# Kernel optimization log

Hardware: AMD Instinct MI355X
Metric: run time of the kernel (lower is better)

Reference implementation:

```python
import jax, jax.numpy as jnp
import numpy as np

N = 50000
IN_DIM = 2000
GRAPH_DIM = 512
HIDDEN_DIM = 256
LATENT_DIM = 64
N_EDGES = 1600000
BN_EPS = 1e-5


def setup_inputs() -> dict:
    key = jax.random.key(0)
    ks = jax.random.split(key, 12)
    x = jax.random.normal(ks[0], (N, IN_DIM), dtype=jnp.float32)
    adj_rows = jax.random.randint(ks[1], (N_EDGES,), 0, N, dtype=jnp.int32)
    adj_cols = jax.random.randint(ks[2], (N_EDGES,), 0, N, dtype=jnp.int32)
    adj_vals = jax.random.uniform(ks[3], (N_EDGES,), dtype=jnp.float32)
    def xavier(k, fan_in, fan_out):
        lim = np.sqrt(6.0 / (fan_in + fan_out)).astype(np.float32)
        return jax.random.uniform(k, (fan_in, fan_out), minval=-lim, maxval=lim, dtype=jnp.float32)
    Wg = xavier(ks[4], IN_DIM, GRAPH_DIM)
    bg = jnp.zeros((GRAPH_DIM,), jnp.float32)
    W1 = xavier(ks[5], GRAPH_DIM, HIDDEN_DIM)
    b1 = jnp.zeros((HIDDEN_DIM,), jnp.float32)
    W21 = xavier(ks[6], HIDDEN_DIM, LATENT_DIM)
    b21 = jnp.zeros((LATENT_DIM,), jnp.float32)
    W22 = xavier(ks[7], HIDDEN_DIM, LATENT_DIM)
    b22 = jnp.zeros((LATENT_DIM,), jnp.float32)
    gamma0 = jnp.ones((GRAPH_DIM,), jnp.float32)
    beta0 = jnp.zeros((GRAPH_DIM,), jnp.float32)
    gamma1 = jnp.ones((HIDDEN_DIM,), jnp.float32)
    beta1 = jnp.zeros((HIDDEN_DIM,), jnp.float32)
    return {"x": x, "adj_rows": adj_rows, "adj_cols": adj_cols, "adj_vals": adj_vals,
            "Wg": Wg, "bg": bg, "W1": W1, "b1": b1, "W21": W21, "b21": b21,
            "W22": W22, "b22": b22, "gamma0": gamma0, "beta0": beta0,
            "gamma1": gamma1, "beta1": beta1}


def batchnorm(h, gamma, beta):
    # training-mode BatchNorm1d: biased variance over batch (node) dim
    mean = jnp.mean(h, axis=0)
    var = jnp.var(h, axis=0)
    return (h - mean) * jax.lax.rsqrt(var + BN_EPS) * gamma + beta


def reference(x, adj_rows, adj_cols, adj_vals, Wg, bg, W1, b1, W21, b21, W22, b22,
              gamma0, beta0, gamma1, beta1):
    # GCN layer: dense projection then sparse aggregation (SpMM via segment_sum)
    h = x @ Wg + bg                                   # [N, GRAPH_DIM]
    msgs = adj_vals[:, None] * h[adj_cols]            # [E, GRAPH_DIM]
    agg = jax.ops.segment_sum(msgs, adj_rows, num_segments=N)
    h0 = jax.nn.softplus(batchnorm(agg, gamma0, beta0))
    h1 = jax.nn.softplus(batchnorm(h0 @ W1 + b1, gamma1, beta1))
    mu = h1 @ W21 + b21
    logvar = h1 @ W22 + b22
    return (mu, logvar)
```

## Files before the change

kernel.cpp:

```cpp
#include <hip/hip_runtime.h>
#include <hip/hip_bf16.h>
#include <stdint.h>

typedef __attribute__((ext_vector_type(8))) short short8;
typedef __attribute__((ext_vector_type(8))) unsigned short ushort8;
typedef __attribute__((ext_vector_type(4))) float f32x4;

#define DEVFN static __device__ __forceinline__

#define NNODES 50000
#define MPAD   50048
#define EDGES  1600000

DEVFN float bf2f(unsigned short u){
  unsigned int v = ((unsigned int)u) << 16;
  return __builtin_bit_cast(float, v);
}
DEVFN unsigned short f2bf(float f){
  unsigned int u = __builtin_bit_cast(unsigned int, f);
  u += 0x7FFFu + ((u >> 16) & 1u);
  return (unsigned short)(u >> 16);
}

typedef __attribute__((address_space(1))) const unsigned int gu32_t;
typedef __attribute__((address_space(3))) unsigned int lu32_t;
DEVFN void async16(const void* g, void* l){
  __builtin_amdgcn_global_load_lds((gu32_t*)g, (lu32_t*)l, 16, 0, 0);
}

__global__ void cast_x_kernel(const float* __restrict__ x, unsigned short* __restrict__ xb){
  long i = (long)blockIdx.x * blockDim.x + threadIdx.x;
  const long total = (long)MPAD * 2048 / 8;
  const long stride = (long)gridDim.x * blockDim.x;
  for (; i < total; i += stride){
    long e0 = i * 8;
    int row = (int)(e0 >> 11);
    int col = (int)(e0 & 2047);
    ushort8 v = {0,0,0,0,0,0,0,0};
    if (row < NNODES && col < 2000){
      const float* s = x + (long)row * 2000 + col;
      #pragma unroll
      for (int j = 0; j < 8; j++) v[j] = f2bf(s[j]);
    }
    *(ushort8*)(xb + e0) = v;
  }
}

__global__ void transpose_cast(const float* __restrict__ src, unsigned short* __restrict__ dst,
                               int K, int Ncols, int Kpad, int rowOff){
  long i = (long)blockIdx.x * blockDim.x + threadIdx.x;
  long total = (long)Ncols * Kpad;
  long stride = (long)gridDim.x * blockDim.x;
  for (; i < total; i += stride){
    int n = (int)(i / Kpad);
    int k = (int)(i - (long)n * Kpad);
    unsigned short v = 0;
    if (k < K) v = f2bf(src[(long)k * Ncols + n]);
    dst[(long)(rowOff + n) * Kpad + k] = v;
  }
}

__global__ void hist_kernel(const int* __restrict__ rows, int* __restrict__ counts){
  int i = blockIdx.x * blockDim.x + threadIdx.x;
  int stride = gridDim.x * blockDim.x;
  for (; i < EDGES; i += stride) atomicAdd(&counts[rows[i]], 1);
}

__global__ void scan_kernel(const int* __restrict__ counts, int* __restrict__ offs){
  __shared__ int part[1024];
  const int n = NNODES;
  const int chunk = 49;
  int t = threadIdx.x;
  int base = t * chunk;
  int s = 0;
  for (int i = 0; i < chunk; i++){ int idx = base + i; if (idx < n) s += counts[idx]; }
  part[t] = s; __syncthreads();
  for (int off = 1; off < 1024; off <<= 1){
    int v = 0;
    if (t >= off) v = part[t - off];
    __syncthreads();
    part[t] += v;
    __syncthreads();
  }
  int run = t ? part[t - 1] : 0;
  for (int i = 0; i < chunk; i++){
    int idx = base + i;
    if (idx <= n){
      offs[idx] = run;
      if (idx < n) run += counts[idx];
    }
  }
}

__global__ void fill_kernel(const int* __restrict__ rows, const int* __restrict__ cols,
                            const float* __restrict__ vals, int* __restrict__ cursor,
                            int* __restrict__ ecol, float* __restrict__ eval){
  int i = blockIdx.x * blockDim.x + threadIdx.x;
  int stride = gridDim.x * blockDim.x;
  for (; i < EDGES; i += stride){
    int r = rows[i];
    int p = atomicAdd(&cursor[r], 1);
    ecol[p] = cols[i];
    eval[p] = vals[i];
  }
}

__launch_bounds__(256)
__global__ void aggregate_kernel(const int* __restrict__ offs, const int* __restrict__ ecol,
                                 const float* __restrict__ eval, const unsigned short* __restrict__ h,
                                 float* __restrict__ agg){
  int wv = threadIdx.x >> 6, lane = threadIdx.x & 63;
  int node = blockIdx.x * 4 + wv;
  int beg = offs[node], end = offs[node + 1];
  float acc[8];
  #pragma unroll
  for (int j = 0; j < 8; j++) acc[j] = 0.f;
  const unsigned short* hp = h + lane * 8;
  for (int i = beg; i < end; i++){
    int c = ecol[i];
    float v = eval[i];
    ushort8 u = *(const ushort8*)(hp + (long)c * 512);
    #pragma unroll
    for (int j = 0; j < 8; j++) acc[j] = fmaf(v, bf2f(u[j]), acc[j]);
  }
  float* op = agg + (long)node * 512 + lane * 8;
  f32x4 lo = {acc[0], acc[1], acc[2], acc[3]};
  f32x4 hi = {acc[4], acc[5], acc[6], acc[7]};
  *(f32x4*)op = lo;
  *(f32x4*)(op + 4) = hi;
}

template<int C>
__global__ void bn_stats_kernel(const float* __restrict__ z, double* __restrict__ dsum, double* __restrict__ dsq){
  constexpr int PC = C / 256;
  int t = threadIdx.x;
  float s[PC], q[PC];
  #pragma unroll
  for (int p = 0; p < PC; p++){ s[p] = 0.f; q[p] = 0.f; }
  for (int r = blockIdx.x; r < NNODES; r += gridDim.x){
    const float* zr = z + (long)r * C;
    #pragma unroll
    for (int p = 0; p < PC; p++){
      float v = zr[t + p * 256];
      s[p] += v; q[p] += v * v;
    }
  }
  #pragma unroll
  for (int p = 0; p < PC; p++){
    atomicAdd(&dsum[t + p * 256], (double)s[p]);
    atomicAdd(&dsq[t + p * 256], (double)q[p]);
  }
}

__global__ void bn_finalize_kernel(const double* __restrict__ dsum, const double* __restrict__ dsq,
                                   const float* __restrict__ gamma, const float* __restrict__ beta,
                                   float* __restrict__ scale, float* __restrict__ shift, int C){
  int c = blockIdx.x * blockDim.x + threadIdx.x;
  if (c < C){
    double m = dsum[c] / (double)NNODES;
    double var = dsq[c] / (double)NNODES - m * m;
    float rs = (float)(1.0 / sqrt(var + 1e-5));
    float sc = rs * gamma[c];
    scale[c] = sc;
    shift[c] = beta[c] - (float)m * sc;
  }
}

template<int C>
__global__ void bn_softplus_kernel(const float* __restrict__ z, const float* __restrict__ scale,
                                   const float* __restrict__ shift, unsigned short* __restrict__ out,
                                   int rowsTotal){
  long i = (long)blockIdx.x * blockDim.x + threadIdx.x;
  long total = (long)rowsTotal * C / 8;
  long stride = (long)gridDim.x * blockDim.x;
  for (; i < total; i += stride){
    long e0 = i * 8;
    int c0 = (int)(e0 & (C - 1));
    const float* zp = z + e0;
    ushort8 o;
    #pragma unroll
    for (int j = 0; j < 8; j++){
      float y = fmaf(zp[j], scale[c0 + j], shift[c0 + j]);
      float sp = (y > 15.f) ? y : log1pf(__expf(y));
      o[j] = f2bf(sp);
    }
    *(ushort8*)(out + e0) = o;
  }
}

template<int EPI>
__launch_bounds__(256, 2)
__global__ void gemm_kernel(const unsigned short* __restrict__ A, const unsigned short* __restrict__ B,
                            const float* __restrict__ bias, const float* __restrict__ bias2,
                            void* __restrict__ Cout, int N, int K){
  __shared__ unsigned short As[128 * 64];
  __shared__ unsigned short Bs[128 * 64];
  const int t = threadIdx.x;
  const int lane = t & 63;
  const int w = t >> 6;
  const long row0 = (long)blockIdx.x * 128;
  const int col0 = blockIdx.y * 128;

  const int rI = lane >> 3;
  const int sI = (lane & 7) ^ rI;

  f32x4 acc[4][4];
  #pragma unroll
  for (int i = 0; i < 4; i++)
    #pragma unroll
    for (int j = 0; j < 4; j++){
      f32x4 z = {0.f, 0.f, 0.f, 0.f};
      acc[i][j] = z;
    }

  const int wm = (w >> 1) * 64;
  const int wn = (w & 1) * 64;
  const int nk = K >> 6;

  const unsigned short* Abase = A + row0 * K + sI * 8;
  const unsigned short* Bbase = B + (long)col0 * K + sI * 8;

  for (int kt = 0; kt < nk; ++kt){
    const int kb = kt * 64;
    #pragma unroll
    for (int i = 0; i < 4; i++){
      int c = i * 4 + w;
      int rowt = c * 8 + rI;
      async16(Abase + (long)rowt * K + kb, As + c * 512);
      async16(Bbase + (long)rowt * K + kb, Bs + c * 512);
    }
    __syncthreads();
    #pragma unroll
    for (int ks = 0; ks < 2; ++ks){
      short8 af[4], bfr[4];
      #pragma unroll
      for (int f = 0; f < 4; f++){
        int ra = wm + f * 16 + (lane & 15);
        int sa = (ks * 4 + (lane >> 4)) ^ (ra & 7);
        af[f] = *(const short8*)(As + ra * 64 + sa * 8);
        int rb = wn + f * 16 + (lane & 15);
        int sb = (ks * 4 + (lane >> 4)) ^ (rb & 7);
        bfr[f] = *(const short8*)(Bs + rb * 64 + sb * 8);
      }
      #pragma unroll
      for (int fm = 0; fm < 4; fm++)
        #pragma unroll
        for (int fn = 0; fn < 4; fn++)
          acc[fm][fn] = __builtin_amdgcn_mfma_f32_16x16x32_bf16(af[fm], bfr[fn], acc[fm][fn], 0, 0, 0);
    }
    __syncthreads();
  }

  #pragma unroll
  for (int fm = 0; fm < 4; fm++){
    #pragma unroll
    for (int fn = 0; fn < 4; fn++){
      #pragma unroll
      for (int j = 0; j < 4; j++){
        long r = row0 + wm + fm * 16 + ((lane >> 4) * 4 + j);
        int cc = col0 + wn + fn * 16 + (lane & 15);
        float v = acc[fm][fn][j];
        if (EPI == 0){
          v += bias[cc];
          ((unsigned short*)Cout)[r * N + cc] = f2bf(v);
        } else if (EPI == 1){
          v += bias[cc];
          ((float*)Cout)[r * N + cc] = v;
        } else {
          if (r < NNODES){
            float bb = (cc < 64) ? bias[cc] : bias2[cc - 64];
            long o = (cc < 64) ? ((long)r * 64 + cc) : ((long)64 * NNODES + (long)r * 64 + (cc - 64));
            ((float*)Cout)[o] = v + bb;
          }
        }
      }
    }
  }
}

extern "C" void kernel_launch(void* const* d_in, const int* in_sizes, int n_in,
                              void* d_out, int out_size, void* d_ws, size_t ws_size,
                              hipStream_t stream){
  const float* x        = (const float*)d_in[0];
  const int*   adj_rows = (const int*)d_in[1];
  const int*   adj_cols = (const int*)d_in[2];
  const float* adj_vals = (const float*)d_in[3];
  const float* Wg       = (const float*)d_in[4];
  const float* bg       = (const float*)d_in[5];
  const float* W1       = (const float*)d_in[6];
  const float* b1       = (const float*)d_in[7];
  const float* W21      = (const float*)d_in[8];
  const float* b21      = (const float*)d_in[9];
  const float* W22      = (const float*)d_in[10];
  const float* b22      = (const float*)d_in[11];
  const float* gamma0   = (const float*)d_in[12];
  const float* beta0    = (const float*)d_in[13];
  const float* gamma1   = (const float*)d_in[14];
  const float* beta1    = (const float*)d_in[15];

  char* ws = (char*)d_ws;
  unsigned short* xb  = (unsigned short*)(ws + 0);
  float* agg          = (float*)(ws + 0);
  float* z1           = (float*)(ws + 102498304);
  unsigned short* h1  = (unsigned short*)(ws + 153747456);
  size_t o = 205000704;
  unsigned short* WgT = (unsigned short*)(ws + o); o += 2097152;
  unsigned short* W1T = (unsigned short*)(ws + o); o += 262144;
  unsigned short* WcT = (unsigned short*)(ws + o); o += 65536;
  unsigned short* hbf = (unsigned short*)(ws + o); o += 51249152;
  unsigned short* h0  = (unsigned short*)(ws + o); o += 51249152;
  int* counts = (int*)(ws + o); o += 200192;
  int* offs   = (int*)(ws + o); o += 200192;
  int* cursor = (int*)(ws + o); o += 200192;
  int* ecol   = (int*)(ws + o); o += 6400000;
  float* eval = (float*)(ws + o); o += 6400000;
  double* dsum0 = (double*)(ws + o); o += 4096;
  double* dsq0  = (double*)(ws + o); o += 4096;
  double* dsum1 = (double*)(ws + o); o += 2048;
  double* dsq1  = (double*)(ws + o); o += 2048;
  float* scale0 = (float*)(ws + o); o += 2048;
  float* shift0 = (float*)(ws + o); o += 2048;
  float* scale1 = (float*)(ws + o); o += 1024;
  float* shift1 = (float*)(ws + o); o += 1024;

  hipMemsetAsync(counts, 0, NNODES * sizeof(int), stream);
  hipMemsetAsync(dsum0, 0, 12288, stream);

  cast_x_kernel<<<2048, 256, 0, stream>>>(x, xb);
  transpose_cast<<<512, 256, 0, stream>>>(Wg, WgT, 2000, 512, 2048, 0);
  transpose_cast<<<128, 256, 0, stream>>>(W1, W1T, 512, 256, 512, 0);
  transpose_cast<<<64, 256, 0, stream>>>(W21, WcT, 256, 64, 256, 0);
  transpose_cast<<<64, 256, 0, stream>>>(W22, WcT, 256, 64, 256, 64);

  hist_kernel<<<2048, 256, 0, stream>>>(adj_rows, counts);
  scan_kernel<<<1, 1024, 0, stream>>>(counts, offs);
  hipMemcpyAsync(cursor, offs, NNODES * sizeof(int), hipMemcpyDeviceToDevice, stream);
  fill_kernel<<<2048, 256, 0, stream>>>(adj_rows, adj_cols, adj_vals, cursor, ecol, eval);

  gemm_kernel<0><<<dim3(MPAD / 128, 4), 256, 0, stream>>>(xb, WgT, bg, nullptr, hbf, 512, 2048);

  aggregate_kernel<<<NNODES / 4, 256, 0, stream>>>(offs, ecol, eval, hbf, agg);

  bn_stats_kernel<512><<<512, 256, 0, stream>>>(agg, dsum0, dsq0);
  bn_finalize_kernel<<<2, 256, 0, stream>>>(dsum0, dsq0, gamma0, beta0, scale0, shift0, 512);
  bn_softplus_kernel<512><<<2048, 256, 0, stream>>>(agg, scale0, shift0, h0, MPAD);

  gemm_kernel<1><<<dim3(MPAD / 128, 2), 256, 0, stream>>>(h0, W1T, b1, nullptr, z1, 256, 512);

  bn_stats_kernel<256><<<512, 256, 0, stream>>>(z1, dsum1, dsq1);
  bn_finalize_kernel<<<1, 256, 0, stream>>>(dsum1, dsq1, gamma1, beta1, scale1, shift1, 256);
  bn_softplus_kernel<256><<<1024, 256, 0, stream>>>(z1, scale1, shift1, h1, MPAD);

  gemm_kernel<2><<<dim3(MPAD / 128, 1), 256, 0, stream>>>(h1, WcT, b21, b22, (float*)d_out, 128, 256);

  (void)in_sizes; (void)n_in; (void)out_size; (void)ws_size;
}
```

Measured before the change: 1.579 ms.

## Parallelize CSR scan, pack edges, unroll aggregation, fuse weight prep

The single-block serial scan becomes a three-kernel parallel scan that also writes the cursor, which removes the device-to-device memcpy. Edge column and value are packed into one 64-bit word, and the aggregation loop is unrolled by four so that four row gathers are in flight at once. The four weight transpose launches are fused into one kernel, and softplus uses a cheaper stable fast-math form. The cost is two extra small scan launches, and the fast log/exp intrinsics give slightly lower precision.

Result: faster. 1.319 ms (-16.4%).

```diff
diff --git a/kernel.cpp b/kernel.cpp
--- a/kernel.cpp
+++ b/kernel.cpp
@@ -11,6 +11,7 @@
 #define NNODES 50000
 #define MPAD   50048
 #define EDGES  1600000
+#define SCHUNK 196
 
 DEVFN float bf2f(unsigned short u){
   unsigned int v = ((unsigned int)u) << 16;
@@ -46,17 +47,33 @@
   }
 }
 
-__global__ void transpose_cast(const float* __restrict__ src, unsigned short* __restrict__ dst,
-                               int K, int Ncols, int Kpad, int rowOff){
-  long i = (long)blockIdx.x * blockDim.x + threadIdx.x;
-  long total = (long)Ncols * Kpad;
-  long stride = (long)gridDim.x * blockDim.x;
+__global__ void prep_weights(const float* __restrict__ Wg, const float* __restrict__ W1,
+                             const float* __restrict__ W21, const float* __restrict__ W22,
+                             unsigned short* __restrict__ WgT, unsigned short* __restrict__ W1T,
+                             unsigned short* __restrict__ WcT){
+  const int n0 = 512 * 2048;
+  const int n1 = 256 * 512;
+  const int n2 = 64 * 256;
+  const int total = n0 + n1 + 2 * n2;
+  int i = blockIdx.x * blockDim.x + threadIdx.x;
+  int stride = gridDim.x * blockDim.x;
   for (; i < total; i += stride){
-    int n = (int)(i / Kpad);
-    int k = (int)(i - (long)n * Kpad);
-    unsigned short v = 0;
-    if (k < K) v = f2bf(src[(long)k * Ncols + n]);
-    dst[(long)(rowOff + n) * Kpad + k] = v;
+    if (i < n0){
+      int n = i >> 11, k = i & 2047;
+      WgT[i] = (k < 2000) ? f2bf(Wg[(long)k * 512 + n]) : (unsigned short)0;
+    } else if (i < n0 + n1){
+      int j = i - n0;
+      int n = j >> 9, k = j & 511;
+      W1T[j] = f2bf(W1[(long)k * 256 + n]);
+    } else if (i < n0 + n1 + n2){
+      int j = i - n0 - n1;
+      int n = j >> 8, k = j & 255;
+      WcT[j] = f2bf(W21[(long)k * 64 + n]);
+    } else {
+      int j = i - n0 - n1 - n2;
+      int n = j >> 8, k = j & 255;
+      WcT[n2 + j] = f2bf(W22[(long)k * 64 + n]);
+    }
   }
 }
 
@@ -66,49 +83,68 @@
   for (; i < EDGES; i += stride) atomicAdd(&counts[rows[i]], 1);
 }
 
-__global__ void scan_kernel(const int* __restrict__ counts, int* __restrict__ offs){
-  __shared__ int part[1024];
-  const int n = NNODES;
-  const int chunk = 49;
+__global__ void scan_partials(const int* __restrict__ counts, int* __restrict__ part){
+  __shared__ int red[256];
+  int b = blockIdx.x, t = threadIdx.x;
+  int idx = b * SCHUNK + t;
+  int s = (t < SCHUNK && idx < NNODES) ? counts[idx] : 0;
+  red[t] = s; __syncthreads();
+  for (int o = 128; o; o >>= 1){
+    if (t < o) red[t] += red[t + o];
+    __syncthreads();
+  }
+  if (!t) part[b] = red[0];
+}
+
+__global__ void scan_scan(int* __restrict__ part){
+  __shared__ int s[256];
   int t = threadIdx.x;
-  int base = t * chunk;
-  int s = 0;
-  for (int i = 0; i < chunk; i++){ int idx = base + i; if (idx < n) s += counts[idx]; }
-  part[t] = s; __syncthreads();
-  for (int off = 1; off < 1024; off <<= 1){
-    int v = 0;
-    if (t >= off) v = part[t - off];
-    __syncthreads();
-    part[t] += v;
-    __syncthreads();
-  }
-  int run = t ? part[t - 1] : 0;
-  for (int i = 0; i < chunk; i++){
-    int idx = base + i;
-    if (idx <= n){
-      offs[idx] = run;
-      if (idx < n) run += counts[idx];
-    }
+  s[t] = part[t]; __syncthreads();
+  for (int o = 1; o < 256; o <<= 1){
+    int v = (t >= o) ? s[t - o] : 0;
+    __syncthreads();
+    s[t] += v;
+    __syncthreads();
+  }
+  part[t] = t ? s[t - 1] : 0;
+}
+
+__global__ void scan_expand(const int* __restrict__ counts, const int* __restrict__ part,
+                            int* __restrict__ offs, int* __restrict__ cursor){
+  __shared__ int s[256];
+  int b = blockIdx.x, t = threadIdx.x;
+  int idx = b * SCHUNK + t;
+  int val = (t < SCHUNK && idx < NNODES) ? counts[idx] : 0;
+  s[t] = val; __syncthreads();
+  for (int o = 1; o < 256; o <<= 1){
+    int v = (t >= o) ? s[t - o] : 0;
+    __syncthreads();
+    s[t] += v;
+    __syncthreads();
+  }
+  if (t < SCHUNK && idx <= NNODES){
+    int excl = s[t] - val + part[b];
+    if (idx < NNODES){ offs[idx] = excl; cursor[idx] = excl; }
+    else offs[NNODES] = excl;
   }
 }
 
 __global__ void fill_kernel(const int* __restrict__ rows, const int* __restrict__ cols,
                             const float* __restrict__ vals, int* __restrict__ cursor,
-                            int* __restrict__ ecol, float* __restrict__ eval){
+                            unsigned long long* __restrict__ ep){
   int i = blockIdx.x * blockDim.x + threadIdx.x;
   int stride = gridDim.x * blockDim.x;
   for (; i < EDGES; i += stride){
     int r = rows[i];
     int p = atomicAdd(&cursor[r], 1);
-    ecol[p] = cols[i];
-    eval[p] = vals[i];
+    unsigned int vb = __builtin_bit_cast(unsigned int, vals[i]);
+    ep[p] = ((unsigned long long)vb << 32) | (unsigned int)cols[i];
   }
 }
 
 __launch_bounds__(256)
-__global__ void aggregate_kernel(const int* __restrict__ offs, const int* __restrict__ ecol,
-                                 const float* __restrict__ eval, const unsigned short* __restrict__ h,
-                                 float* __restrict__ agg){
+__global__ void aggregate_kernel(const int* __restrict__ offs, const unsigned long long* __restrict__ ep,
+                                 const unsigned short* __restrict__ h, float* __restrict__ agg){
   int wv = threadIdx.x >> 6, lane = threadIdx.x & 63;
   int node = blockIdx.x * 4 + wv;
   int beg = offs[node], end = offs[node + 1];
@@ -116,10 +152,29 @@
   #pragma unroll
   for (int j = 0; j < 8; j++) acc[j] = 0.f;
   const unsigned short* hp = h + lane * 8;
-  for (int i = beg; i < end; i++){
-    int c = ecol[i];
-    float v = eval[i];
-    ushort8 u = *(const ushort8*)(hp + (long)c * 512);
+  int i = beg;
+  for (; i + 4 <= end; i += 4){
+    unsigned long long e0 = ep[i], e1 = ep[i + 1], e2 = ep[i + 2], e3 = ep[i + 3];
+    const ushort8 u0 = *(const ushort8*)(hp + (long)(unsigned int)e0 * 512);
+    const ushort8 u1 = *(const ushort8*)(hp + (long)(unsigned int)e1 * 512);
+    const ushort8 u2 = *(const ushort8*)(hp + (long)(unsigned int)e2 * 512);
+    const ushort8 u3 = *(const ushort8*)(hp + (long)(unsigned int)e3 * 512);
+    float v0 = __builtin_bit_cast(float, (unsigned int)(e0 >> 32));
+    float v1 = __builtin_bit_cast(float, (unsigned int)(e1 >> 32));
+    float v2 = __builtin_bit_cast(float, (unsigned int)(e2 >> 32));
+    float v3 = __builtin_bit_cast(float, (unsigned int)(e3 >> 32));
+    #pragma unroll
+    for (int j = 0; j < 8; j++){
+      acc[j] = fmaf(v0, bf2f(u0[j]), acc[j]);
+      acc[j] = fmaf(v1, bf2f(u1[j]), acc[j]);
+      acc[j] = fmaf(v2, bf2f(u2[j]), acc[j]);
+      acc[j] = fmaf(v3, bf2f(u3[j]), acc[j]);
+    }
+  }
+  for (; i < end; i++){
+    unsigned long long e = ep[i];
+    const ushort8 u = *(const ushort8*)(hp + (long)(unsigned int)e * 512);
+    float v = __builtin_bit_cast(float, (unsigned int)(e >> 32));
     #pragma unroll
     for (int j = 0; j < 8; j++) acc[j] = fmaf(v, bf2f(u[j]), acc[j]);
   }
@@ -181,7 +236,7 @@
     #pragma unroll
     for (int j = 0; j < 8; j++){
       float y = fmaf(zp[j], scale[c0 + j], shift[c0 + j]);
-      float sp = (y > 15.f) ? y : log1pf(__expf(y));
+      float sp = fmaxf(y, 0.f) + __logf(1.f + __expf(-fabsf(y)));
       o[j] = f2bf(sp);
     }
     *(ushort8*)(out + e0) = o;
@@ -312,8 +367,7 @@
   int* counts = (int*)(ws + o); o += 200192;
   int* offs   = (int*)(ws + o); o += 200192;
   int* cursor = (int*)(ws + o); o += 200192;
-  int* ecol   = (int*)(ws + o); o += 6400000;
-  float* eval = (float*)(ws + o); o += 6400000;
+  unsigned long long* ep = (unsigned long long*)(ws + o); o += 12800000;
   double* dsum0 = (double*)(ws + o); o += 4096;
   double* dsq0  = (double*)(ws + o); o += 4096;
   double* dsum1 = (double*)(ws + o); o += 2048;
@@ -322,24 +376,23 @@
   float* shift0 = (float*)(ws + o); o += 2048;
   float* scale1 = (float*)(ws + o); o += 1024;
   float* shift1 = (float*)(ws + o); o += 1024;
+  int* part     = (int*)(ws + o); o += 1024;
 
   hipMemsetAsync(counts, 0, NNODES * sizeof(int), stream);
   hipMemsetAsync(dsum0, 0, 12288, stream);
 
   cast_x_kernel<<<2048, 256, 0, stream>>>(x, xb);
-  transpose_cast<<<512, 256, 0, stream>>>(Wg, WgT, 2000, 512, 2048, 0);
-  transpose_cast<<<128, 256, 0, stream>>>(W1, W1T, 512, 256, 512, 0);
-  transpose_cast<<<64, 256, 0, stream>>>(W21, WcT, 256, 64, 256, 0);
-  transpose_cast<<<64, 256, 0, stream>>>(W22, WcT, 256, 64, 256, 64);
+  prep_weights<<<1184, 256, 0, stream>>>(Wg, W1, W21, W22, WgT, W1T, WcT);
 
   hist_kernel<<<2048, 256, 0, stream>>>(adj_rows, counts);
-  scan_kernel<<<1, 1024, 0, stream>>>(counts, offs);
-  hipMemcpyAsync(cursor, offs, NNODES * sizeof(int), hipMemcpyDeviceToDevice, stream);
-  fill_kernel<<<2048, 256, 0, stream>>>(adj_rows, adj_cols, adj_vals, cursor, ecol, eval);
+  scan_partials<<<256, 256, 0, stream>>>(counts, part);
+  scan_scan<<<1, 256, 0, stream>>>(part);
+  scan_expand<<<256, 256, 0, stream>>>(counts, part, offs, cursor);
+  fill_kernel<<<2048, 256, 0, stream>>>(adj_rows, adj_cols, adj_vals, cursor, ep);
 
   gemm_kernel<0><<<dim3(MPAD / 128, 4), 256, 0, stream>>>(xb, WgT, bg, nullptr, hbf, 512, 2048);
 
-  aggregate_kernel<<<NNODES / 4, 256, 0, stream>>>(offs, ecol, eval, hbf, agg);
+  aggregate_kernel<<<NNODES / 4, 256, 0, stream>>>(offs, ep, hbf, agg);
 
   bn_stats_kernel<512><<<512, 256, 0, stream>>>(agg, dsum0, dsq0);
   bn_finalize_kernel<<<2, 256, 0, stream>>>(dsum0, dsq0, gamma0, beta0, scale0, shift0, 512);
```
